# Kernel optimization log

Measured on AMD Instinct MI355X. Metric: run time of the kernel, lower is better.

Reference implementation:

```python
import jax, jax.numpy as jnp
import numpy as np

N, E, M, NC, G = 20000, 640000, 200000, 50000, 512
VOCAB, IN, HID, OUT, NCLS = 8, 64, 128, 128, 2
EPS = 1e-5
SLOPE = 0.01


def _bn(x, g, b):
    # BatchNorm1d in training mode: biased batch statistics (matches torch normalization)
    m = jnp.mean(x, axis=0)
    v = jnp.var(x, axis=0)
    return g * (x - m) * jax.lax.rsqrt(v + EPS) + b


def _seg_softmax(a, ids, ns):
    m = jax.ops.segment_max(a, ids, num_segments=ns)
    ex = jnp.exp(a - m[ids])
    s = jax.ops.segment_sum(ex, ids, num_segments=ns)
    return ex / s[ids]


def _seg_mean(x, ids, ns):
    s = jax.ops.segment_sum(x, ids, num_segments=ns)
    c = jax.ops.segment_sum(jnp.ones((x.shape[0], 1), x.dtype), ids, num_segments=ns)
    return s / jnp.maximum(c, 1.0)


def setup_inputs() -> dict:
    key = jax.random.key(0)
    ks = jax.random.split(key, 24)

    def nrm(k, shape, fan_in):
        return jax.random.normal(k, shape, jnp.float32) * np.float32(1.0 / np.sqrt(fan_in))

    inp = {
        "sub_x": jax.random.randint(ks[0], (N, 1), 0, VOCAB),
        "sub_edge_index": jax.random.randint(ks[1], (2, E), 0, N),
        "batch": jnp.sort(jax.random.randint(ks[2], (N,), 0, G)),
        "cycle_seg_id": jnp.sort(jax.random.randint(ks[3], (M,), 0, NC)),
        "cycle_edge_idx": jax.random.randint(ks[4], (M,), 0, E),
        # embedding + mlp_feature (nn.Linear with bias)
        "emb": nrm(ks[5], (VOCAB, IN), 1),
        "w1": nrm(ks[6], (2 * IN, 2 * IN), 2 * IN), "b1": jnp.zeros((2 * IN,), jnp.float32),
        "w2": nrm(ks[7], (2 * IN, HID), 2 * IN), "b2": jnp.zeros((HID,), jnp.float32),
        "g0": jnp.ones((HID,), jnp.float32), "beta0": jnp.zeros((HID,), jnp.float32),
        # bond_agg_layer (bias-free linears)
        "watt_b": nrm(ks[8], (HID,), HID),
        "wb1": nrm(ks[9], (HID, OUT), HID), "wb2": nrm(ks[10], (OUT, OUT), OUT),
        "g1": jnp.ones((OUT,), jnp.float32), "beta1": jnp.zeros((OUT,), jnp.float32),
        # cycle_agg_layer
        "watt_c": nrm(ks[11], (HID,), HID),
        "wc1": nrm(ks[12], (HID, OUT), HID), "wc2": nrm(ks[13], (OUT, OUT), OUT),
        "g2": jnp.ones((OUT,), jnp.float32), "beta2": jnp.zeros((OUT,), jnp.float32),
        # edge_agg_layer
        "we1": nrm(ks[14], (HID, OUT), HID), "we2": nrm(ks[15], (OUT, OUT), OUT),
        "wl1": nrm(ks[16], (OUT, OUT), OUT), "wl2": nrm(ks[17], (OUT, OUT), OUT),
        "g3": jnp.ones((OUT,), jnp.float32), "beta3": jnp.zeros((OUT,), jnp.float32),
        # graph_agg_layer
        "wg1": nrm(ks[18], (OUT, OUT), OUT), "wg2": nrm(ks[19], (OUT, OUT), OUT),
        "g4": jnp.ones((OUT,), jnp.float32), "beta4": jnp.zeros((OUT,), jnp.float32),
        "wout": nrm(ks[20], (OUT, NCLS), OUT),
    }
    return inp


def reference(sub_x, sub_edge_index, batch, cycle_seg_id, cycle_edge_idx,
              emb, w1, b1, w2, b2, g0, beta0,
              watt_b, wb1, wb2, g1, beta1,
              watt_c, wc1, wc2, g2, beta2,
              we1, we2, wl1, wl2, g3, beta3,
              wg1, wg2, g4, beta4, wout):
    src, dst = sub_edge_index[0], sub_edge_index[1]
    x0 = emb[sub_x[:, 0]]                                    # [N, IN]
    h = jnp.concatenate([x0[src], x0[dst]], axis=-1)         # [E, 2*IN]
    h = (h @ w1 + b1) @ w2 + b2                              # [E, HID]
    h = jax.nn.gelu(_bn(h, g0, beta0), approximate=False)
    # bond aggregation: per-target-node segment softmax attention + scatter-mean
    ab = jax.nn.leaky_relu(h @ watt_b, SLOPE)                # [E]
    ab = _seg_softmax(ab, dst, N)
    bond = _seg_mean(ab[:, None] * h, dst, N)                # [N, HID]
    bond = jax.nn.gelu(_bn((bond @ wb1) @ wb2, g1, beta1), approximate=False)
    # cycle aggregation over membership list (cycle_seg_id: cycle id, cycle_edge_idx: edge idx)
    hc = h[cycle_edge_idx]                                   # [M, HID]
    ac = jax.nn.leaky_relu(hc @ watt_c, SLOPE)               # [M]
    ac = _seg_softmax(ac, cycle_seg_id, NC)
    cyc = _seg_mean(ac[:, None] * hc, cycle_seg_id, NC)      # [NC, HID]
    cyc = jax.nn.gelu(_bn((cyc @ wc1) @ wc2, g2, beta2), approximate=False)
    # edge update
    e = (h @ we1) @ we2                                      # [E, OUT]
    xc = jax.ops.segment_sum(cyc[cycle_seg_id], cycle_edge_idx, num_segments=E)
    e = ((e + bond[src] + bond[dst] + xc) @ wl1) @ wl2
    e = jax.nn.gelu(_bn(e, g3, beta3), approximate=False)
    # graph readout: sum edges by graph of their source node
    gsum = jax.ops.segment_sum(e, batch[src], num_segments=G)  # [G, OUT]
    gsum = (gsum @ wg1) @ wg2
    gsum = jax.nn.gelu(_bn(gsum, g4, beta4), approximate=False)
    return gsum @ wout                                       # [G, NCLS]
```

## Files before the change

kernel.cpp:

```cpp
#include <hip/hip_runtime.h>
#include <hip/hip_bf16.h>

typedef __hip_bfloat16 bf16;
typedef __attribute__((ext_vector_type(4))) float f32x4;
typedef __attribute__((ext_vector_type(8))) short bf16x8;

__device__ __forceinline__ float b2f(bf16 v){ return __bfloat162float(v); }
__device__ __forceinline__ bf16  f2b(float v){ return __float2bfloat16(v); }
__device__ __forceinline__ float erf_fast(float x){
  const float ax=fabsf(x);
  const float t=__builtin_amdgcn_rcpf(1.f+0.3275911f*ax);
  const float p=t*(0.254829592f+t*(-0.284496736f+t*(1.421413741f+t*(-1.453152027f+t*1.061405429f))));
  const float r=1.f-p*__expf(-ax*ax);
  return copysignf(r,x);
}
__device__ __forceinline__ float geluf(float x){ return 0.5f*x*(1.0f+erf_fast(x*0.70710678118654752f)); }
__device__ __forceinline__ float lreluf(float x){ return x>0.f? x : 0.01f*x; }
__device__ __forceinline__ float bflo(unsigned u){ return __builtin_bit_cast(float,(unsigned)((u&0xFFFFu)<<16)); }
__device__ __forceinline__ float bfhi(unsigned u){ return __builtin_bit_cast(float,(unsigned)(u&0xFFFF0000u)); }
__device__ __forceinline__ unsigned packbf(float a, float b){
  bf16 ha=f2b(a), hb=f2b(b);
  return (unsigned)__builtin_bit_cast(unsigned short,ha) | ((unsigned)__builtin_bit_cast(unsigned short,hb)<<16);
}

__device__ __forceinline__ int detect_bf16(const unsigned int* words){
  int hits=0;
  for(int i=0;i<64;i++){
    unsigned u=words[i], lo=u&0xFFFFu, e=(lo>>7)&0xFFu;
    if(lo==0u || (e>=100u && e<=140u)) hits++;
  }
  return (hits>=40)?1:0;
}

struct ConvertArgs { const void* src[28]; float* dst[28]; int n[28]; };
__global__ __launch_bounds__(256) void k_convert(ConvertArgs A, const unsigned int* embw,
                                                 int* flag, float* zp, int zn){
  const int id=blockIdx.x;
  if(id<28){
    const int bf=detect_bf16(embw);
    if(id==0 && threadIdx.x==0) *flag=bf;
    const void* s=A.src[id];
    float* d=A.dst[id];
    const int n=A.n[id];
    if(bf){
      const bf16* sp=(const bf16*)s;
      for(int i=threadIdx.x;i<n;i+=256) d[i]=b2f(sp[i]);
    } else {
      const float* sp=(const float*)s;
      for(int i=threadIdx.x;i<n;i+=256) d[i]=sp[i];
    }
  } else {
    const int zb=id-28;
    int i=zb*256+threadIdx.x;
    const int stride=1024*256;
    for(;i<zn;i+=stride) zp[i]=0.f;
  }
}

struct GemmTasks5 { const float* X[5]; const float* W[5]; float* Y[5]; };

template<int K>
__global__ __launch_bounds__(256) void k_rowgemm(GemmTasks5 T5, int rows, int mode, int xPacked,
    const float* stS, const float* stQ, float invRows,
    const float* gam, const float* bet,
    float* outS, float* outQ, unsigned* Yp, const float* partsIn)
{
  constexpr int KH = K/2;
  const int task = blockIdx.y;
  const float* Xv = T5.X[task];
  const float* W  = T5.W[task];
  float* Y = T5.Y[task];
  const int tid = threadIdx.x, c = tid & 127, kh = tid >> 7;
  __shared__ float redSQ[256];
  if(mode==1 && partsIn){
    float s=0.f;
    for(int k=0;k<64;k++) s+=partsIn[k*256+tid];
    redSQ[tid]=s;
    __syncthreads();
  }
  float wreg[KH];
  #pragma unroll
  for(int i=0;i<KH;i++) wreg[i]=W[(kh*KH+i)*128+c];
  __shared__ float xls[8*K];
  __shared__ float part[2*8*128];
  float ls=0.f, lq=0.f;
  const int nbatch=(rows+7)>>3;
  for (int b=blockIdx.x; b<nbatch; b+=gridDim.x){
    const int base=b*8;
    for (int idx=tid; idx<8*K; idx+=256){
      const int row=idx/K, k=idx-row*K, r=base+row;
      float v=0.f;
      if (r<rows){
        if(xPacked){
          const unsigned u=((const unsigned*)Xv)[(size_t)r*(K/2)+(k>>1)];
          v = (k&1) ? bfhi(u) : bflo(u);
        } else {
          v = Xv[(size_t)r*K+k];
        }
        if (mode==1){
          const float sv = partsIn ? redSQ[k]     : stS[k];
          const float qv = partsIn ? redSQ[128+k] : stQ[k];
          float mn=sv*invRows;
          float vr=fmaxf(qv*invRows-mn*mn,0.f);
          float sc=gam[k]*rsqrtf(vr+1e-5f);
          float sh=bet[k]-mn*sc;
          v=geluf(v*sc+sh);
        }
      }
      xls[idx]=v;
    }
    __syncthreads();
    #pragma unroll
    for (int rr=0;rr<8;rr++){
      const float* xp=&xls[rr*K+kh*KH];
      float acc=0.f;
      #pragma unroll
      for (int j=0;j<KH;j+=4){
        const float4 xv=*(const float4*)(xp+j);
        acc += wreg[j]*xv.x + wreg[j+1]*xv.y + wreg[j+2]*xv.z + wreg[j+3]*xv.w;
      }
      part[kh*1024 + rr*128 + c]=acc;
    }
    __syncthreads();
    if (Yp==nullptr){
      #pragma unroll
      for (int q=0;q<4;q++){
        const int r=kh*4+q, row=base+r;
        if (row<rows){
          float y=part[r*128+c]+part[1024+r*128+c];
          Y[row*128+c]=y;
          ls+=y; lq+=y*y;
        }
      }
      __syncthreads();
    } else {
      if constexpr (K==128){
        #pragma unroll
        for (int q=0;q<4;q++){
          const int r=kh*4+q, row=base+r;
          float y=0.f;
          if (row<rows){
            y=part[r*128+c]+part[1024+r*128+c];
            ls+=y; lq+=y*y;
          }
          xls[r*128+c]=y;
        }
        __syncthreads();
        for (int idx=tid; idx<512; idx+=256){
          const int r2=idx>>6, j=idx&63, row=base+r2;
          if(row<rows) Yp[(size_t)row*64+j]=packbf(xls[r2*128+2*j],xls[r2*128+2*j+1]);
        }
        __syncthreads();
      }
    }
  }
  if (outS){ atomicAdd(&outS[c],ls); atomicAdd(&outQ[c],lq); }
}

struct RGDual {
  const float* x0; int rows0; int pk0; float inv0; const float* g0; const float* b0;
  unsigned* yp0; const float* parts0;
  const float* x1; int rows1; int pk1; float inv1; const float* g1; const float* b1;
  unsigned* yp1; const float* parts1;
  const float* W;
};
__global__ __launch_bounds__(256) void k_rowgemm_dual(RGDual D)
{
  const int tid=threadIdx.x;
  const int lane=tid&63, wave=tid>>6;
  const int l15=lane&15, lhi=lane>>4;
  __shared__ float scs0[128], shs0[128], scs1[128], shs1[128];
  {
    const int t=tid>>7, k=tid&127;
    const float* partsIn = t ? D.parts1 : D.parts0;
    float s=0.f,q=0.f;
    for(int j=0;j<64;j++){ s+=partsIn[j*256+k]; }
    for(int j=0;j<64;j++){ q+=partsIn[j*256+128+k]; }
    const float invRows = t ? D.inv1 : D.inv0;
    const float gam = (t ? D.g1 : D.g0)[k];
    const float bet = (t ? D.b1 : D.b0)[k];
    const float mn=s*invRows;
    const float vr=fmaxf(q*invRows-mn*mn,0.f);
    const float sc=gam*rsqrtf(vr+1e-5f);
    const float sh=bet-mn*sc;
    if(t){ scs1[k]=sc; shs1[k]=sh; } else { scs0[k]=sc; shs0[k]=sh; }
  }
  bf16x8 breg[2][4];
  #pragma unroll
  for(int ct=0;ct<2;ct++){
    const int col=(wave*2+ct)*16 + l15;
    #pragma unroll
    for(int ks=0;ks<4;ks++){
      const int kb=ks*32 + lhi*8;
      #pragma unroll
      for(int i=0;i<8;i++){
        breg[ct][ks][i]=__builtin_bit_cast(short, f2b(D.W[(size_t)(kb+i)*128+col]));
      }
    }
  }
  __syncthreads();
  __shared__ short xtile[16*136];
  const int TB0=(D.rows0+15)>>4, TB1=(D.rows1+15)>>4;
  const int TBT=TB0+TB1;
  for (int gb=blockIdx.x; gb<TBT; gb+=gridDim.x){
    const int t1=(gb>=TB0);
    const int b = t1 ? gb-TB0 : gb;
    const float* Xv = t1 ? D.x1 : D.x0;
    const int rows  = t1 ? D.rows1 : D.rows0;
    const int xPacked = t1 ? D.pk1 : D.pk0;
    unsigned* Yp = t1 ? D.yp1 : D.yp0;
    const float* scs = t1 ? scs1 : scs0;
    const float* shs = t1 ? shs1 : shs0;
    const int base=b*16;
    for (int idx=tid; idx<1024; idx+=256){
      const int row=idx>>6, kp=idx&63, k0=kp*2, r=base+row;
      float v0=0.f,v1=0.f;
      if (r<rows){
        if(xPacked){
          const unsigned u=((const unsigned*)Xv)[(size_t)r*64+kp];
          v0=bflo(u); v1=bfhi(u);
        } else {
          const float2 xv=((const float2*)(Xv+(size_t)r*128))[kp];
          v0=xv.x; v1=xv.y;
        }
        v0=geluf(v0*scs[k0]+shs[k0]);
        v1=geluf(v1*scs[k0+1]+shs[k0+1]);
      }
      ((unsigned*)xtile)[row*68+kp]=packbf(v0,v1);
    }
    __syncthreads();
    f32x4 acc0={0.f,0.f,0.f,0.f}, acc1={0.f,0.f,0.f,0.f};
    #pragma unroll
    for(int ks=0;ks<4;ks++){
      const bf16x8 afrag = *reinterpret_cast<const bf16x8*>(&xtile[l15*136 + ks*32 + lhi*8]);
      acc0=__builtin_amdgcn_mfma_f32_16x16x32_bf16(afrag,breg[0][ks],acc0,0,0,0);
      acc1=__builtin_amdgcn_mfma_f32_16x16x32_bf16(afrag,breg[1][ks],acc1,0,0,0);
    }
    #pragma unroll
    for(int j=0;j<4;j++){
      const int row=base+lhi*4+j;
      const float ya=acc0[j];
      const float ya2=__shfl_xor(ya,1,64);
      if(((lane&1)==0) && row<rows)
        Yp[(size_t)row*64 + (wave*2+0)*8 + (l15>>1)]=packbf(ya,ya2);
      const float yb=acc1[j];
      const float yb2=__shfl_xor(yb,1,64);
      if(((lane&1)==0) && row<rows)
        Yp[(size_t)row*64 + (wave*2+1)*8 + (l15>>1)]=packbf(yb,yb2);
    }
    __syncthreads();
  }
}

__global__ __launch_bounds__(256) void k_table_T(const float* emb, const float* w1, const float* b1,
                                                 const float* w2, const float* b2, float* T)
{
  __shared__ float A[2048];
  const int tid=threadIdx.x;
  for (int idx=tid; idx<2048; idx+=256){
    const int half=idx>>10, rem=idx&1023, s=rem>>7, j=rem&127;
    float acc=0.f;
    for(int k=0;k<64;k++) acc += emb[s*64+k]*w1[(half*64+k)*128+j];
    A[idx]=acc;
  }
  __syncthreads();
  const int o=tid&127;
  for(int rr=tid>>7; rr<8; rr+=2){
    const int r=blockIdx.x*8+rr, s=r>>3, d=r&7;
    float acc=b2[o];
    for(int j=0;j<128;j++){
      float t1=A[s*128+j]+A[1024+d*128+j]+b1[j];
      acc+=t1*w2[j*128+o];
    }
    T[r*128+o]=acc;
  }
}

#define SCH 1024

__global__ __launch_bounds__(256) void k_edge_code(const int* sx, const int* src, const int* dst,
    const int* batch, unsigned char* code, unsigned short* gg, int* cnt64, int* ns,
    int* blockHist, int E)
{
  __shared__ int hist[64];
  __shared__ int gh[512];
  const int tid=threadIdx.x;
  if(tid<64) hist[tid]=0;
  for(int i=tid;i<512;i+=256) gh[i]=0;
  __syncthreads();
  const int base=blockIdx.x*SCH;
  #pragma unroll
  for(int u=0;u<SCH/256;u++){
    const int e=base+u*256+tid;
    if(e<E){
      const int s_=src[e], d_=dst[e];
      const int sc=sx[s_], dc=sx[d_];
      const int cd=sc*8+dc;
      code[e]=(unsigned char)cd;
      const int gb=batch[s_];
      gg[e]=(unsigned short)gb;
      atomicAdd(&hist[cd],1);
      atomicAdd(&ns[d_*8+sc],1);
      atomicAdd(&gh[gb],1);
    }
  }
  __syncthreads();
  if(tid<64){ int h=hist[tid]; if(h) atomicAdd(&cnt64[tid],h); }
  for(int i=tid;i<512;i+=256) blockHist[blockIdx.x*512+i]=gh[i];
}

__global__ __launch_bounds__(256) void k_gscan_col(int* blockHist, int* gtot, int NB){
  const int g=blockIdx.x;
  const int tid=threadIdx.x;
  __shared__ int sd[256];
  int run=0;
  for(int base=0;base<NB;base+=256){
    const int b=base+tid;
    const int v=(b<NB)?blockHist[(size_t)b*512+g]:0;
    sd[tid]=v; __syncthreads();
    for(int d=1;d<256;d<<=1){ int t=(tid>=d)?sd[tid-d]:0; __syncthreads(); sd[tid]+=t; __syncthreads(); }
    const int incl=sd[tid];
    const int tot=sd[255];
    if(b<NB) blockHist[(size_t)b*512+g]=run+incl-v;
    __syncthreads();
    run+=tot;
  }
  if(tid==0) gtot[g]=run;
}

__global__ __launch_bounds__(256) void k_gscatter(const unsigned short* gg, const int* blockHist,
    const int* gtot, const unsigned char* code, const int* src, const int* dst,
    unsigned short* sortedG, int* posE, unsigned long long* recP, int E){
  __shared__ int baseg[512];
  __shared__ int sg[512];
  const int tid=threadIdx.x;
  for(int i=tid;i<512;i+=256) sg[i]=gtot[i];
  __syncthreads();
  for(int d=1;d<512;d<<=1){
    int t0[2];
    for(int i=tid,j=0;i<512;i+=256,j++) t0[j]=(i>=d)?sg[i-d]:0;
    __syncthreads();
    for(int i=tid,j=0;i<512;i+=256,j++) sg[i]+=t0[j];
    __syncthreads();
  }
  for(int i=tid;i<512;i+=256) baseg[i]=blockHist[blockIdx.x*512+i]+sg[i]-gtot[i];
  __syncthreads();
  const int base=blockIdx.x*SCH;
  for(int i=tid;i<SCH;i+=256){
    const int e=base+i;
    if(e<E){
      const int g=gg[e];
      const int p=atomicAdd(&baseg[g],1);
      sortedG[p]=(unsigned short)g;
      posE[e]=p;
      recP[p]=(unsigned long long)code[e] | ((unsigned long long)(unsigned)src[e]<<8)
            | ((unsigned long long)(unsigned)dst[e]<<32);
    }
  }
}

__global__ __launch_bounds__(256) void k_htable(const float* T, const int* cnt64,
    const float* g0, const float* beta0, const float* wattb, const float* wattc,
    float* h_table, float* abt, float* act, float* ea, int E)
{
  __shared__ float h[64*132];
  __shared__ float cw[64];
  const int tid=threadIdx.x;
  if(tid<64) cw[tid]=(float)cnt64[tid];
  __syncthreads();
  const int c=tid&127;
  const float invE=1.f/(float)E;
  float s=0.f,q=0.f;
  for(int r2=0;r2<64;r2++){ float v=T[r2*128+c]; float w=cw[r2]; s+=w*v; q+=w*v*v; }
  const float mn=s*invE, vr=fmaxf(q*invE-mn*mn,0.f);
  const float sc=g0[c]*rsqrtf(vr+1e-5f), sh=beta0[c]-mn*sc;
  for(int r=tid>>7; r<64; r+=2){
    float v=geluf(T[r*128+c]*sc+sh);
    h[r*132+c]=v;
    h_table[r*128+c]=v;
  }
  __syncthreads();
  if(tid<64){
    float sb=0.f,scc=0.f;
    for(int k=0;k<128;k++){ float hv=h[tid*132+k]; sb+=hv*wattb[k]; scc+=hv*wattc[k]; }
    const float ab_=lreluf(sb), ac_=lreluf(scc);
    abt[tid]=ab_; act[tid]=ac_;
    float mx=ac_;
    #pragma unroll
    for(int o=1;o<64;o<<=1) mx=fmaxf(mx,__shfl_xor(mx,o,64));
    ea[tid]=expf(ac_-mx);
  }
}

__global__ __launch_bounds__(256) void k_cycle_hist(const int* cseg, const int* cidx,
    const unsigned char* code, const int* posE, int* nsc, int* cntP, int M)
{
  const int base=blockIdx.x*1024+threadIdx.x;
  #pragma unroll
  for(int u=0;u<4;u++){
    const int m=base+u*256;
    if(m<M){
      const int e=cidx[m];
      atomicAdd(&nsc[cseg[m]*64 + (int)code[e]],1);
      atomicAdd(&cntP[posE[e]],1);
    }
  }
}

__global__ __launch_bounds__(256) void k_bond(const int* ns, const int* sx, const float* abt,
    const float* hWb, float* bm, float* parts, int N)
{
  const int tid=threadIdx.x, c=tid&127, grp=tid>>7;
  float ls=0.f,lq=0.f;
  const int base=blockIdx.x*16+grp*8;
  for(int i=0;i<8;i++){
    const int n=base+i;
    if(n>=N) break;
    const int d=sx[n];
    float cnt=0.f, mx=-1e30f, nsv[8];
    #pragma unroll
    for(int s=0;s<8;s++){ float v=(float)ns[n*8+s]; nsv[s]=v; cnt+=v; if(v>0.f) mx=fmaxf(mx,abt[s*8+d]); }
    float y=0.f;
    if(cnt>0.f){
      float ssum=0.f, ex[8];
      #pragma unroll
      for(int s=0;s<8;s++){ ex[s]= nsv[s]>0.f ? nsv[s]*expf(abt[s*8+d]-mx) : 0.f; ssum+=ex[s]; }
      const float inv=1.f/(ssum*cnt);
      #pragma unroll
      for(int s=0;s<8;s++){ if(ex[s]>0.f) y += (ex[s]*inv)*hWb[(s*8+d)*128+c]; }
    }
    bm[n*128+c]=y;
    ls+=y; lq+=y*y;
  }
  __shared__ float sS[128], sQ[128];
  if(tid<128){ sS[tid]=0.f; sQ[tid]=0.f; }
  __syncthreads();
  atomicAdd(&sS[c],ls); atomicAdd(&sQ[c],lq);
  __syncthreads();
  if(tid<128){
    float* slot=&parts[(size_t)(blockIdx.x&63)*256];
    atomicAdd(&slot[tid],sS[tid]); atomicAdd(&slot[128+tid],sQ[tid]);
  }
}

__global__ __launch_bounds__(256) void k_cyc(const int* nsc, const float* ea,
    const float* hWc, unsigned* ucm, float* parts, int NC)
{
  const int tid=threadIdx.x, c=tid&127, kh=tid>>7;
  const int lane=tid&63;
  const int wv4=tid>>6;
  const float eaL=ea[lane];
  float wreg[32];
  #pragma unroll
  for(int i=0;i<32;i++) wreg[i]=hWc[(kh*32+i)*128+c]*ea[kh*32+i];
  __shared__ float cnts[512];
  __shared__ float part[2*8*128];
  __shared__ float invcs[8];
  float ls=0.f,lq=0.f;
  const int nbatch=(NC+7)>>3;
  for(int b=blockIdx.x;b<nbatch;b+=gridDim.x){
    const int base=b*8;
    for(int i=tid;i<512;i+=256){
      const int seg=base+(i>>6);
      cnts[i] = (seg<NC) ? (float)nsc[(size_t)seg*64+(i&63)] : 0.f;
    }
    __syncthreads();
    #pragma unroll
    for(int rr2=0;rr2<2;rr2++){
      const int r=wv4*2+rr2;
      const float n=cnts[r*64+lane];
      float S=n*eaL, C=n;
      #pragma unroll
      for(int o=1;o<64;o<<=1){ S+=__shfl_xor(S,o,64); C+=__shfl_xor(C,o,64); }
      if(lane==0) invcs[r]=(C>0.f&&S>0.f)?1.f/(S*C):0.f;
    }
    #pragma unroll
    for(int rr=0;rr<8;rr++){
      const float* xp=&cnts[rr*64+kh*32];
      float acc=0.f;
      #pragma unroll
      for(int j=0;j<32;j+=4){
        const float4 xv=*(const float4*)(xp+j);
        acc += wreg[j]*xv.x + wreg[j+1]*xv.y + wreg[j+2]*xv.z + wreg[j+3]*xv.w;
      }
      part[kh*1024+rr*128+c]=acc;
    }
    __syncthreads();
    #pragma unroll
    for(int q=0;q<4;q++){
      const int r=kh*4+q, row=base+r;
      float y=0.f;
      if(row<NC){
        y=(part[r*128+c]+part[1024+r*128+c])*invcs[r];
        ls+=y; lq+=y*y;
      }
      const float y2=__shfl_xor(y,1,64);
      if(((lane&1)==0) && row<NC) ucm[(size_t)row*64+(c>>1)]=packbf(y,y2);
    }
    __syncthreads();
  }
  __shared__ float sS[128], sQ[128];
  if(tid<128){ sS[tid]=0.f; sQ[tid]=0.f; }
  __syncthreads();
  atomicAdd(&sS[c],ls); atomicAdd(&sQ[c],lq);
  __syncthreads();
  if(tid<128){
    float* slot=&parts[(size_t)(blockIdx.x&63)*256];
    atomicAdd(&slot[tid],sS[tid]); atomicAdd(&slot[128+tid],sQ[tid]);
  }
}

__global__ __launch_bounds__(256) void k_scan_block(const int* cntP, int* blkSum, int E){
  __shared__ int sd[256];
  const int tid=threadIdx.x, base=blockIdx.x*1024;
  int s=0;
  for(int q=0;q<4;q++){ int i=base+tid*4+q; if(i<E) s+=cntP[i]; }
  sd[tid]=s; __syncthreads();
  for(int d=1;d<256;d<<=1){ int t=(tid>=d)?sd[tid-d]:0; __syncthreads(); sd[tid]+=t; __syncthreads(); }
  if(tid==255) blkSum[blockIdx.x]=sd[255];
}

__global__ __launch_bounds__(256) void k_scan_mid(const int* blkSum, int* blkOff, int nb){
  __shared__ int sd[1024];
  const int tid=threadIdx.x;
  for(int i=tid;i<1024;i+=256) sd[i]=(i<nb)?blkSum[i]:0;
  __syncthreads();
  for(int d=1;d<1024;d<<=1){
    int t[4];
    for(int i=tid,j=0;i<1024;i+=256,j++) t[j]=(i>=d)?sd[i-d]:0;
    __syncthreads();
    for(int i=tid,j=0;i<1024;i+=256,j++) sd[i]+=t[j];
    __syncthreads();
  }
  for(int i=tid;i<nb;i+=256) blkOff[i]=sd[i]-blkSum[i];
}

__global__ __launch_bounds__(256) void k_scan_write(const int* cntP, const int* blkOff,
                                                    int* offP, int E, int M){
  __shared__ int sd[256];
  const int tid=threadIdx.x, base=blockIdx.x*1024;
  int v[4]; int s=0;
  for(int q=0;q<4;q++){ int i=base+tid*4+q; v[q]=(i<E)?cntP[i]:0; s+=v[q]; }
  sd[tid]=s; __syncthreads();
  for(int d=1;d<256;d<<=1){ int t=(tid>=d)?sd[tid-d]:0; __syncthreads(); sd[tid]+=t; __syncthreads(); }
  int run=blkOff[blockIdx.x]+sd[tid]-s;
  for(int q=0;q<4;q++){ int i=base+tid*4+q; if(i<E) offP[i]=run; run+=v[q]; }
  if(blockIdx.x==0&&tid==0) offP[E]=M;
}

__global__ __launch_bounds__(256) void k_place(const int* cseg, const int* cidx, const int* posE,
                                               const int* offP, int* cursor, int* entrySeg, int M){
  const int base=blockIdx.x*1024+threadIdx.x;
  #pragma unroll
  for(int u=0;u<4;u++){
    const int m=base+u*256;
    if(m<M){
      const int p=posE[cidx[m]];
      const int pos=offP[p]+atomicAdd(&cursor[p],1);
      entrySeg[pos]=cseg[m];
    }
  }
}

__global__ __launch_bounds__(256) void k_pass1_store(const unsigned long long* recP,
    const float* eLt, const unsigned* ubond, const unsigned* ucyc,
    const int* offP, const int* entrySeg, unsigned* vbuf, float* parts,
    int E, int upx)
{
  const int tid=threadIdx.x;
  const int lane=tid&63, wave=tid>>6;
  const int xcd=blockIdx.x&7;
  const int wix=(blockIdx.x>>3)*4+wave;
  const int NU=(E+15)>>4;
  int u0=xcd*upx + (int)(((long long)wix*(long long)upx)>>10);
  int u1=xcd*upx + (int)(((long long)(wix+1)*(long long)upx)>>10);
  if(u0>NU)u0=NU; if(u1>NU)u1=NU;
  int e=u0*16; const int e1=(u1*16<E)?u1*16:E;
  float lsx=0.f,lsy=0.f,lqx=0.f,lqy=0.f;
  while(e<e1){
    int nv=e1-e; if(nv>64)nv=64;
    const int t=e+((lane<nv)?lane:(nv-1));
    const unsigned long long r0=recP[t];
    const unsigned rlo=(unsigned)r0, rhi=(unsigned)(r0>>32);
    const int oa0=offP[t], ob0=offP[t+1];
    int i=0;
    for(; i+8<=nv; i+=8){
      unsigned lo[8],hi[8]; int a[8],b[8];
      #pragma unroll
      for(int q=0;q<8;q++){
        lo[q]=(unsigned)__builtin_amdgcn_readlane((int)rlo,i+q);
        hi[q]=(unsigned)__builtin_amdgcn_readlane((int)rhi,i+q);
        a[q]=__builtin_amdgcn_readlane(oa0,i+q);
        b[q]=__builtin_amdgcn_readlane(ob0,i+q);
      }
      float2 ea[8]; unsigned ub[8],ud[8];
      #pragma unroll
      for(int q=0;q<8;q++){
        ea[q]=((const float2*)(eLt+(size_t)(lo[q]&0xFFu)*128))[lane];
        ub[q]=ubond[(size_t)(lo[q]>>8)*64+lane];
        ud[q]=ubond[(size_t)hi[q]*64+lane];
      }
      #pragma unroll
      for(int q=0;q<8;q++){
        float x=ea[q].x+bflo(ub[q])+bflo(ud[q]);
        float y=ea[q].y+bfhi(ub[q])+bfhi(ud[q]);
        for(int j=a[q];j<b[q];j++){
          const unsigned w=ucyc[(size_t)entrySeg[j]*64+lane];
          x+=bflo(w); y+=bfhi(w);
        }
        lsx+=x; lqx+=x*x; lsy+=y; lqy+=y*y;
        vbuf[(size_t)(e+i+q)*64+lane]=packbf(x,y);
      }
    }
    for(; i<nv; i++){
      const unsigned lo=(unsigned)__builtin_amdgcn_readlane((int)rlo,i);
      const unsigned hi=(unsigned)__builtin_amdgcn_readlane((int)rhi,i);
      const int a=__builtin_amdgcn_readlane(oa0,i);
      const int b=__builtin_amdgcn_readlane(ob0,i);
      const float2 ea2=((const float2*)(eLt+(size_t)(lo&0xFFu)*128))[lane];
      const unsigned ub=ubond[(size_t)(lo>>8)*64+lane];
      const unsigned ud=ubond[(size_t)hi*64+lane];
      float x=ea2.x+bflo(ub)+bflo(ud);
      float y=ea2.y+bfhi(ub)+bfhi(ud);
      for(int j=a;j<b;j++){
        const unsigned w=ucyc[(size_t)entrySeg[j]*64+lane];
        x+=bflo(w); y+=bfhi(w);
      }
      lsx+=x; lqx+=x*x; lsy+=y; lqy+=y*y;
      vbuf[(size_t)(e+i)*64+lane]=packbf(x,y);
    }
    e+=nv;
  }
  __shared__ float sS[128], sQ[128];
  if(tid<128){ sS[tid]=0.f; sQ[tid]=0.f; }
  __syncthreads();
  const int c0=lane*2;
  atomicAdd(&sS[c0],lsx); atomicAdd(&sS[c0+1],lsy);
  atomicAdd(&sQ[c0],lqx); atomicAdd(&sQ[c0+1],lqy);
  __syncthreads();
  if(tid<128){
    float* slot=&parts[(size_t)(blockIdx.x&63)*256];
    atomicAdd(&slot[tid],sS[tid]); atomicAdd(&slot[128+tid],sQ[tid]);
  }
}

__global__ __launch_bounds__(256) void k_pass2_stream(const unsigned* vbuf1,
    const int* gtot, const float* parts,
    const float* g3, const float* beta3, float* gsum, int E)
{
  __shared__ float sSQ[256];
  __shared__ int sg[512];
  __shared__ int goffL[513];
  const int tid=threadIdx.x;
  {
    float s=0.f;
    #pragma unroll 8
    for(int k=0;k<64;k++) s+=parts[k*256+tid];
    sSQ[tid]=s;
  }
  for(int i=tid;i<512;i+=256) sg[i]=gtot[i];
  __syncthreads();
  for(int d=1;d<512;d<<=1){
    int t0[2];
    for(int i=tid,j=0;i<512;i+=256,j++) t0[j]=(i>=d)?sg[i-d]:0;
    __syncthreads();
    for(int i=tid,j=0;i<512;i+=256,j++) sg[i]+=t0[j];
    __syncthreads();
  }
  for(int i=tid;i<512;i+=256) goffL[i]=sg[i]-gtot[i];
  if(tid==0) goffL[512]=E;
  __syncthreads();
  const int lane=tid&63, wave=tid>>6;
  const int c0=lane*2;
  const float invE=1.f/(float)E;
  float mn=sSQ[c0]*invE, vr=fmaxf(sSQ[128+c0]*invE-mn*mn,0.f);
  const float sc0=g3[c0]*rsqrtf(vr+1e-5f), sh0=beta3[c0]-mn*sc0;
  mn=sSQ[c0+1]*invE; vr=fmaxf(sSQ[128+c0+1]*invE-mn*mn,0.f);
  const float sc1=g3[c0+1]*rsqrtf(vr+1e-5f), sh1=beta3[c0+1]-mn*sc1;
  const int wix=blockIdx.x*4+wave;
  int i0=(int)(((long long)wix*(long long)E)>>13);
  int i1=(int)(((long long)(wix+1)*(long long)E)>>13);
  if(i1>E)i1=E;
  if(i0>=i1) return;
  int glo=0, ghi=512;
  while(glo+1<ghi){ const int gm=(glo+ghi)>>1; if(goffL[gm]<=i0) glo=gm; else ghi=gm; }
  int g=glo;
  int i=i0;
  while(i<i1){
    const int segEnd = (goffL[g+1]<i1)?goffL[g+1]:i1;
    if(segEnd<=i){ g++; continue; }
    float a0=0.f,a1=0.f;
    for(; i+16<=segEnd; i+=16){
      unsigned uq[16];
      #pragma unroll
      for(int q=0;q<16;q++) uq[q]=vbuf1[(size_t)(i+q)*64+lane];
      #pragma unroll
      for(int q=0;q<16;q++){
        a0+=geluf(fmaf(bflo(uq[q]),sc0,sh0));
        a1+=geluf(fmaf(bfhi(uq[q]),sc1,sh1));
      }
    }
    for(; i+4<=segEnd; i+=4){
      unsigned uq[4];
      #pragma unroll
      for(int q=0;q<4;q++) uq[q]=vbuf1[(size_t)(i+q)*64+lane];
      #pragma unroll
      for(int q=0;q<4;q++){
        a0+=geluf(fmaf(bflo(uq[q]),sc0,sh0));
        a1+=geluf(fmaf(bfhi(uq[q]),sc1,sh1));
      }
    }
    for(; i<segEnd; i++){
      const unsigned u=vbuf1[(size_t)i*64+lane];
      a0+=geluf(fmaf(bflo(u),sc0,sh0));
      a1+=geluf(fmaf(bfhi(u),sc1,sh1));
    }
    atomicAdd(&gsum[g*128+c0],a0); atomicAdd(&gsum[g*128+c0+1],a1);
    g++;
  }
}

__global__ __launch_bounds__(256) void k_out(const float* gw, const float* st4S, const float* st4Q,
    const float* g4, const float* beta4, const float* wout, void* out, const int* flag, int G)
{
  const int lane=threadIdx.x&63;
  const int r=blockIdx.x*4 + (threadIdx.x>>6);
  const float invG=1.f/(float)G;
  float a0=0.f,a1=0.f;
  #pragma unroll
  for(int h=0;h<2;h++){
    const int k=lane+64*h;
    const float mn=st4S[k]*invG;
    const float vr=fmaxf(st4Q[k]*invG-mn*mn,0.f);
    const float sc=g4[k]*rsqrtf(vr+1e-5f), sh=beta4[k]-mn*sc;
    const float v=geluf(gw[r*128+k]*sc+sh);
    a0+=v*wout[k*2+0]; a1+=v*wout[k*2+1];
  }
  for(int o=1;o<64;o<<=1){ a0+=__shfl_xor(a0,o,64); a1+=__shfl_xor(a1,o,64); }
  if(lane==0){
    if(*flag){ ((bf16*)out)[r*2+0]=f2b(a0); ((bf16*)out)[r*2+1]=f2b(a1); }
    else     { ((float*)out)[r*2+0]=a0;     ((float*)out)[r*2+1]=a1; }
  }
}

extern "C" void kernel_launch(void* const* d_in, const int* in_sizes, int n_in,
                              void* d_out, int out_size, void* d_ws, size_t ws_size,
                              hipStream_t stream)
{
  const int N  = in_sizes[0];
  const int E  = in_sizes[1]/2;
  const int M  = in_sizes[3];
  const int NC = 50000;
  const int G  = 512;

  const int* sub_x=(const int*)d_in[0];
  const int* src=(const int*)d_in[1];
  const int* dst=src+E;
  const int* batch=(const int*)d_in[2];
  const int* cseg=(const int*)d_in[3];
  const int* cidx=(const int*)d_in[4];

  char* ws=(char*)d_ws;
  size_t off=0;
  auto carve=[&](size_t bytes)->char*{ char* p=ws+off; off=(off+bytes+255)&~(size_t)255; return p; };

  size_t ftot=0;
  for(int i=0;i<28;i++) ftot += (size_t)in_sizes[5+i];
  float* stage=(float*)carve(ftot*4);
  float* fin[28];
  { size_t so=0; for(int i=0;i<28;i++){ fin[i]=stage+so; so+=(size_t)in_sizes[5+i]; } }
  const float *emb_f=fin[0], *w1_f=fin[1], *b1_f=fin[2], *w2_f=fin[3], *b2_f=fin[4],
              *g0_f=fin[5], *beta0_f=fin[6], *wattb_f=fin[7], *wb1_f=fin[8], *wb2_f=fin[9],
              *g1_f=fin[10], *beta1_f=fin[11], *wattc_f=fin[12], *wc1_f=fin[13], *wc2_f=fin[14],
              *g2_f=fin[15], *beta2_f=fin[16], *we1_f=fin[17], *we2_f=fin[18], *wl1_f=fin[19],
              *wl2_f=fin[20], *g3_f=fin[21], *beta3_f=fin[22], *wg1_f=fin[23], *wg2_f=fin[24],
              *g4_f=fin[25], *beta4_f=fin[26], *wout_f=fin[27];

  int* flag=(int*)carve(256);
  float* Wb =(float*)carve(65536);
  float* Wc =(float*)carve(65536);
  float* Wl =(float*)carve(65536);
  float* Wg =(float*)carve(65536);
  float* We =(float*)carve(65536);
  float* Wel=(float*)carve(65536);
  float* T      =(float*)carve(64*128*4);
  float* h_table=(float*)carve(64*128*4);
  float* hWb    =(float*)carve(64*128*4);
  float* hWc    =(float*)carve(64*128*4);
  float* eLt    =(float*)carve(64*128*4);
  float* abt=(float*)carve(256);
  float* act=(float*)carve(256);
  float* eaT=(float*)carve(256);
  float* bm   =(float*)carve((size_t)N*128*4);
  unsigned* ucm=(unsigned*)carve((size_t)NC*64*4);
  unsigned* ubond=(unsigned*)carve((size_t)N*64*4);
  unsigned* ucyc =(unsigned*)carve((size_t)NC*64*4);
  unsigned char* code=(unsigned char*)carve((size_t)E);
  unsigned short* gg=(unsigned short*)carve((size_t)E*2);
  unsigned short* sortedG=(unsigned short*)carve((size_t)E*2);
  int*   posE  =(int*)carve((size_t)E*4);
  unsigned long long* recP=(unsigned long long*)carve((size_t)E*8);
  int*   offP  =(int*)carve((size_t)(E+1)*4);
  int*   entrySeg=(int*)carve((size_t)M*4);
  int*   blkSum=(int*)carve(4096);
  int*   blkOff=(int*)carve(4096);
  int*   gtot  =(int*)carve(2048);
  const int NB=(E+SCH-1)/SCH;
  int*   blockHist=(int*)carve((size_t)NB*512*4);
  float* gw  =(float*)carve((size_t)G*128*4);

  const size_t zStart=off;
  int*   cnt64=(int*)carve(256);
  float* stats=(float*)carve(4096);
  float* st4S=stats+6*128, *st4Q=stats+7*128;
  float* parts1=(float*)carve(64*256*4);
  float* parts2=(float*)carve(64*256*4);
  float* parts3=(float*)carve(64*256*4);
  float* gsum=(float*)carve((size_t)G*128*4);
  int*   ns   =(int*)carve((size_t)N*8*4);
  int*   nsc  =(int*)carve((size_t)NC*64*4);
  int*   cntP =(int*)carve((size_t)E*4);
  int*   cursor=(int*)carve((size_t)E*4);
  const size_t zEnd=off;

  unsigned* vbuf=(unsigned*)carve((size_t)E*64*4);
  const int haveV = (off <= ws_size) ? 1 : 0;
  (void)n_in; (void)out_size;

  {
    ConvertArgs A{};
    for(int i=0;i<28;i++){ A.src[i]=d_in[5+i]; A.dst[i]=fin[i]; A.n[i]=in_sizes[5+i]; }
    k_convert<<<28+1024,256,0,stream>>>(A,(const unsigned int*)d_in[5],flag,
                                        (float*)(ws+zStart),(int)((zEnd-zStart)/4));
  }

  k_table_T<<<8,256,0,stream>>>(emb_f,w1_f,b1_f,w2_f,b2_f,T);

  {
    GemmTasks5 t{};
    t.X[0]=wb1_f; t.W[0]=wb2_f; t.Y[0]=Wb;
    t.X[1]=wc1_f; t.W[1]=wc2_f; t.Y[1]=Wc;
    t.X[2]=wl1_f; t.W[2]=wl2_f; t.Y[2]=Wl;
    t.X[3]=wg1_f; t.W[3]=wg2_f; t.Y[3]=Wg;
    t.X[4]=we1_f; t.W[4]=we2_f; t.Y[4]=We;
    k_rowgemm<128><<<dim3(16,5),256,0,stream>>>(t,128,0,0,nullptr,nullptr,0.f,nullptr,nullptr,nullptr,nullptr,nullptr,nullptr);
  }
  {
    GemmTasks5 t{};
    t.X[0]=We; t.W[0]=Wl; t.Y[0]=Wel;
    k_rowgemm<128><<<dim3(16,1),256,0,stream>>>(t,128,0,0,nullptr,nullptr,0.f,nullptr,nullptr,nullptr,nullptr,nullptr,nullptr);
  }

  k_edge_code<<<NB,256,0,stream>>>(sub_x,src,dst,batch,code,gg,cnt64,ns,blockHist,E);
  k_gscan_col<<<512,256,0,stream>>>(blockHist,gtot,NB);
  k_gscatter<<<NB,256,0,stream>>>(gg,blockHist,gtot,code,src,dst,sortedG,posE,recP,E);
  k_htable<<<1,256,0,stream>>>(T,cnt64,g0_f,beta0_f,wattb_f,wattc_f,h_table,abt,act,eaT,E);
  {
    GemmTasks5 t{};
    t.X[0]=h_table; t.W[0]=Wb;  t.Y[0]=hWb;
    t.X[1]=h_table; t.W[1]=Wc;  t.Y[1]=hWc;
    t.X[2]=h_table; t.W[2]=Wel; t.Y[2]=eLt;
    k_rowgemm<128><<<dim3(8,3),256,0,stream>>>(t,64,0,0,nullptr,nullptr,0.f,nullptr,nullptr,nullptr,nullptr,nullptr,nullptr);
  }
  k_cycle_hist<<<(M+1023)/1024,256,0,stream>>>(cseg,cidx,code,posE,nsc,cntP,M);
  k_bond<<<(N+15)/16,256,0,stream>>>(ns,sub_x,abt,hWb,bm,parts1,N);
  k_cyc<<<2048,256,0,stream>>>(nsc,eaT,hWc,ucm,parts2,NC);
  {
    RGDual D{};
    D.x0=bm;                 D.rows0=N;  D.pk0=0; D.inv0=1.f/(float)N;  D.g0=g1_f; D.b0=beta1_f; D.yp0=ubond; D.parts0=parts1;
    D.x1=(const float*)ucm;  D.rows1=NC; D.pk1=1; D.inv1=1.f/(float)NC; D.g1=g2_f; D.b1=beta2_f; D.yp1=ucyc;  D.parts1=parts2;
    D.W=Wl;
    k_rowgemm_dual<<<2048,256,0,stream>>>(D);
  }
  const int nb=(E+1023)/1024;
  k_scan_block<<<nb,256,0,stream>>>(cntP,blkSum,E);
  k_scan_mid<<<1,256,0,stream>>>(blkSum,blkOff,nb);
  k_scan_write<<<nb,256,0,stream>>>(cntP,blkOff,offP,E,M);
  k_place<<<(M+1023)/1024,256,0,stream>>>(cseg,cidx,posE,offP,cursor,entrySeg,M);
  {
    const int NU=(E+15)/16;
    const int upx=(NU+7)/8;
    k_pass1_store<<<2048,256,0,stream>>>(recP,eLt,ubond,ucyc,offP,entrySeg,
                                         haveV?vbuf:(unsigned*)cursor,parts3,E,upx);
    k_pass2_stream<<<2048,256,0,stream>>>(vbuf,gtot,parts3,
                                          g3_f,beta3_f,gsum,E);
  }
  {
    GemmTasks5 t{};
    t.X[0]=gsum; t.W[0]=Wg; t.Y[0]=gw;
    k_rowgemm<128><<<dim3(64,1),256,0,stream>>>(t,G,0,0,nullptr,nullptr,0.f,nullptr,nullptr,st4S,st4Q,nullptr,nullptr);
  }
  k_out<<<G/4,256,0,stream>>>(gw,st4S,st4Q,g4_f,beta4_f,wout_f,d_out,flag,G);
}
```

Measured before the change: 549.6 us.

## Use bf16 MFMA for cycle aggregation GEMM and drop unused sortedG writes

Rewrites k_cyc to process 16-row tiles with bf16 16x16x32 MFMA instructions, holding pre-scaled weight fragments in registers instead of doing fp32 FMA dot products with a shared partial-sum reduction. It also removes the sortedG store from the group scatter kernel because that buffer is no longer consumed. The MFMA path rounds counts and weights to bf16, which adds some precision loss in exchange for less ALU work and shared-memory traffic.

```diff
diff --git a/kernel.cpp b/kernel.cpp
--- a/kernel.cpp
+++ b/kernel.cpp
@@ -330,7 +330,7 @@
 
 __global__ __launch_bounds__(256) void k_gscatter(const unsigned short* gg, const int* blockHist,
     const int* gtot, const unsigned char* code, const int* src, const int* dst,
-    unsigned short* sortedG, int* posE, unsigned long long* recP, int E){
+    int* posE, unsigned long long* recP, int E){
   __shared__ int baseg[512];
   __shared__ int sg[512];
   const int tid=threadIdx.x;
@@ -351,7 +351,6 @@
     if(e<E){
       const int g=gg[e];
       const int p=atomicAdd(&baseg[g],1);
-      sortedG[p]=(unsigned short)g;
       posE[e]=p;
       recP[p]=(unsigned long long)code[e] | ((unsigned long long)(unsigned)src[e]<<8)
             | ((unsigned long long)(unsigned)dst[e]<<32);
@@ -446,63 +445,75 @@
 __global__ __launch_bounds__(256) void k_cyc(const int* nsc, const float* ea,
     const float* hWc, unsigned* ucm, float* parts, int NC)
 {
-  const int tid=threadIdx.x, c=tid&127, kh=tid>>7;
-  const int lane=tid&63;
-  const int wv4=tid>>6;
+  const int tid=threadIdx.x;
+  const int lane=tid&63, wave=tid>>6;
+  const int l15=lane&15, lhi=lane>>4;
+  bf16x8 breg[2][2];
+  #pragma unroll
+  for(int ct=0;ct<2;ct++){
+    const int col=(wave*2+ct)*16+l15;
+    #pragma unroll
+    for(int ks=0;ks<2;ks++){
+      const int kb=ks*32+lhi*8;
+      #pragma unroll
+      for(int i=0;i<8;i++)
+        breg[ct][ks][i]=__builtin_bit_cast(short, f2b(hWc[(size_t)(kb+i)*128+col]*ea[kb+i]));
+    }
+  }
+  __shared__ float cnts[16*64];
+  __shared__ short atile[16*72];
+  __shared__ float invcs[16];
+  __shared__ float sS[128], sQ[128];
+  if(tid<128){ sS[tid]=0.f; sQ[tid]=0.f; }
   const float eaL=ea[lane];
-  float wreg[32];
-  #pragma unroll
-  for(int i=0;i<32;i++) wreg[i]=hWc[(kh*32+i)*128+c]*ea[kh*32+i];
-  __shared__ float cnts[512];
-  __shared__ float part[2*8*128];
-  __shared__ float invcs[8];
-  float ls=0.f,lq=0.f;
-  const int nbatch=(NC+7)>>3;
-  for(int b=blockIdx.x;b<nbatch;b+=gridDim.x){
-    const int base=b*8;
-    for(int i=tid;i<512;i+=256){
+  float ls0=0.f,lq0=0.f,ls1=0.f,lq1=0.f;
+  const int ntile=(NC+15)>>4;
+  for(int b=blockIdx.x;b<ntile;b+=gridDim.x){
+    const int base=b*16;
+    __syncthreads();
+    for(int i=tid;i<1024;i+=256){
       const int seg=base+(i>>6);
-      cnts[i] = (seg<NC) ? (float)nsc[(size_t)seg*64+(i&63)] : 0.f;
+      const float v=(seg<NC)?(float)nsc[(size_t)seg*64+(i&63)]:0.f;
+      cnts[i]=v;
+      atile[(i>>6)*72+(i&63)]=__builtin_bit_cast(short,f2b(v));
     }
     __syncthreads();
     #pragma unroll
-    for(int rr2=0;rr2<2;rr2++){
-      const int r=wv4*2+rr2;
+    for(int rr2=0;rr2<4;rr2++){
+      const int r=wave*4+rr2;
       const float n=cnts[r*64+lane];
       float S=n*eaL, C=n;
       #pragma unroll
       for(int o=1;o<64;o<<=1){ S+=__shfl_xor(S,o,64); C+=__shfl_xor(C,o,64); }
       if(lane==0) invcs[r]=(C>0.f&&S>0.f)?1.f/(S*C):0.f;
     }
+    f32x4 acc0={0.f,0.f,0.f,0.f}, acc1={0.f,0.f,0.f,0.f};
     #pragma unroll
-    for(int rr=0;rr<8;rr++){
-      const float* xp=&cnts[rr*64+kh*32];
-      float acc=0.f;
-      #pragma unroll
-      for(int j=0;j<32;j+=4){
-        const float4 xv=*(const float4*)(xp+j);
-        acc += wreg[j]*xv.x + wreg[j+1]*xv.y + wreg[j+2]*xv.z + wreg[j+3]*xv.w;
-      }
-      part[kh*1024+rr*128+c]=acc;
+    for(int ks=0;ks<2;ks++){
+      const bf16x8 afrag=*reinterpret_cast<const bf16x8*>(&atile[l15*72+ks*32+lhi*8]);
+      acc0=__builtin_amdgcn_mfma_f32_16x16x32_bf16(afrag,breg[0][ks],acc0,0,0,0);
+      acc1=__builtin_amdgcn_mfma_f32_16x16x32_bf16(afrag,breg[1][ks],acc1,0,0,0);
     }
     __syncthreads();
     #pragma unroll
-    for(int q=0;q<4;q++){
-      const int r=kh*4+q, row=base+r;
-      float y=0.f;
-      if(row<NC){
-        y=(part[r*128+c]+part[1024+r*128+c])*invcs[r];
-        ls+=y; lq+=y*y;
-      }
-      const float y2=__shfl_xor(y,1,64);
-      if(((lane&1)==0) && row<NC) ucm[(size_t)row*64+(c>>1)]=packbf(y,y2);
-    }
-    __syncthreads();
-  }
-  __shared__ float sS[128], sQ[128];
-  if(tid<128){ sS[tid]=0.f; sQ[tid]=0.f; }
-  __syncthreads();
-  atomicAdd(&sS[c],ls); atomicAdd(&sQ[c],lq);
+    for(int j=0;j<4;j++){
+      const int r16=lhi*4+j, row=base+r16;
+      const float iv=invcs[r16];
+      const float y0=acc0[j]*iv;
+      const float y1=acc1[j]*iv;
+      ls0+=y0; lq0+=y0*y0; ls1+=y1; lq1+=y1*y1;
+      const float y0b=__shfl_xor(y0,1,64);
+      if(((lane&1)==0) && row<NC)
+        ucm[(size_t)row*64 + (wave*2+0)*8 + (l15>>1)]=packbf(y0,y0b);
+      const float y1b=__shfl_xor(y1,1,64);
+      if(((lane&1)==0) && row<NC)
+        ucm[(size_t)row*64 + (wave*2+1)*8 + (l15>>1)]=packbf(y1,y1b);
+    }
+  }
+  __syncthreads();
+  const int c0=(wave*2+0)*16+l15, c1=(wave*2+1)*16+l15;
+  atomicAdd(&sS[c0],ls0); atomicAdd(&sQ[c0],lq0);
+  atomicAdd(&sS[c1],ls1); atomicAdd(&sQ[c1],lq1);
   __syncthreads();
   if(tid<128){
     float* slot=&parts[(size_t)(blockIdx.x&63)*256];
@@ -825,7 +836,7 @@
 
   unsigned* vbuf=(unsigned*)carve((size_t)E*64*4);
   const int haveV = (off <= ws_size) ? 1 : 0;
-  (void)n_in; (void)out_size;
+  (void)n_in; (void)out_size; (void)sortedG;
 
   {
     ConvertArgs A{};
@@ -853,7 +864,7 @@
 
   k_edge_code<<<NB,256,0,stream>>>(sub_x,src,dst,batch,code,gg,cnt64,ns,blockHist,E);
   k_gscan_col<<<512,256,0,stream>>>(blockHist,gtot,NB);
-  k_gscatter<<<NB,256,0,stream>>>(gg,blockHist,gtot,code,src,dst,sortedG,posE,recP,E);
+  k_gscatter<<<NB,256,0,stream>>>(gg,blockHist,gtot,code,src,dst,posE,recP,E);
   k_htable<<<1,256,0,stream>>>(T,cnt64,g0_f,beta0_f,wattb_f,wattc_f,h_table,abt,act,eaT,E);
   {
     GemmTasks5 t{};
```

After: 536.9 us. 2.3% less time.
